# Performance work log

Measured on AMD Instinct MI355X. Metric: run time of the kernel, lower is better.

The kernel has to match this reference:

```python
import jax, jax.numpy as jnp
import numpy as np

SEQ, B, IN, H = 512, 64, 1024, 1024

def _lstm_layer(x_seq, Wx, bx, Wh, bh):
    # x_seq: [S, B, D], Wx: [4H, D], Wh: [4H, H]
    h0 = jnp.zeros((x_seq.shape[1], Wh.shape[1]), x_seq.dtype)
    c0 = jnp.zeros_like(h0)
    def step(carry, x_t):
        h, c = carry
        z = x_t @ Wx.T + bx + h @ Wh.T + bh  # [B, 4H]
        i, f, g, o = jnp.split(z, 4, axis=1)
        c1 = jax.nn.sigmoid(f) * c + jax.nn.sigmoid(i) * jnp.tanh(g)
        h1 = jax.nn.sigmoid(o) * jnp.tanh(c1)
        return (h1, c1), h1
    _, hs = jax.lax.scan(step, (h0, c0), x_seq)
    return hs  # [S, B, H]

def setup_inputs() -> dict:
    key = jax.random.key(0)
    ks = jax.random.split(key, 9)
    s_in = 1.0 / np.sqrt(IN)
    s_h = 1.0 / np.sqrt(H)
    return {
        "x": jax.random.normal(ks[0], (SEQ, B, IN), jnp.float32),
        "Wx0": jax.random.uniform(ks[1], (4 * H, IN), jnp.float32, -s_in, s_in),
        "bx0": jax.random.uniform(ks[2], (4 * H,), jnp.float32, -s_in, s_in),
        "Wh0": jax.random.uniform(ks[3], (4 * H, H), jnp.float32, -s_h, s_h),
        "bh0": jax.random.uniform(ks[4], (4 * H,), jnp.float32, -s_h, s_h),
        "Wx1": jax.random.uniform(ks[5], (4 * H, H), jnp.float32, -s_h, s_h),
        "bx1": jax.random.uniform(ks[6], (4 * H,), jnp.float32, -s_h, s_h),
        "Wh1": jax.random.uniform(ks[7], (4 * H, H), jnp.float32, -s_h, s_h),
        "bh1": jax.random.uniform(ks[8], (4 * H,), jnp.float32, -s_h, s_h),
    }

def reference(x, Wx0, bx0, Wh0, bh0, Wx1, bx1, Wh1, bh1):
    # Two stacked unidirectional LSTM layers, zero initial states.
    h_seq0 = _lstm_layer(x, Wx0, bx0, Wh0, bh0)
    h_seq1 = _lstm_layer(h_seq0, Wx1, bx1, Wh1, bh1)
    return h_seq1  # [S, B, H] = stacked version of the torch list output
```

## Files before the change

kernel.cpp:

```cpp
#include <hip/hip_runtime.h>


#define SEQ   512
#define BATCH 64
#define HID   1024
#define NG    4096
#define KCAT  2048
#define F0_BASE 0
#define E0_IDX  8192
#define F1_BASE 16384
#define E1_IDX  24576

#define SMEM_BYTES 133120

typedef __attribute__((ext_vector_type(8))) _Float16 f16x8;
typedef __attribute__((ext_vector_type(4))) _Float16 f16x4;
typedef __attribute__((ext_vector_type(4))) float    f32x4;

__device__ __forceinline__ float sigm_f(float x){ return 1.f/(1.f + __expf(-x)); }
__device__ __forceinline__ float tanh_f(float x){
    float e = __expf(-2.f*fabsf(x));
    float r = (1.f - e)/(1.f + e);
    return copysignf(r, x);
}

__device__ __forceinline__ void store_h8(_Float16* p, f16x4 v){
    asm volatile("global_store_dwordx2 %0, %1, off sc0 sc1" :: "v"(p), "v"(v) : "memory");
}
__device__ __forceinline__ void drain_vmem(){
    asm volatile("s_waitcnt vmcnt(0)" ::: "memory");
}

#define GLD(dst, base, OFF) \
    asm volatile("global_load_dwordx4 %0, %1, off offset:" #OFF \
                 : "=&v"(dst) : "v"(base))
#define GLD8L(arr, i, B) \
    GLD(arr[(i)+0],B,0);   GLD(arr[(i)+1],B,64);  GLD(arr[(i)+2],B,128); GLD(arr[(i)+3],B,192); \
    GLD(arr[(i)+4],B,256); GLD(arr[(i)+5],B,320); GLD(arr[(i)+6],B,384); GLD(arr[(i)+7],B,448)
#define GLD8H(arr, i, B) \
    GLD(arr[(i)+0],B,512); GLD(arr[(i)+1],B,576); GLD(arr[(i)+2],B,640); GLD(arr[(i)+3],B,704); \
    GLD(arr[(i)+4],B,768); GLD(arr[(i)+5],B,832); GLD(arr[(i)+6],B,896); GLD(arr[(i)+7],B,960)
#define VMWAIT0 \
    asm volatile("s_waitcnt vmcnt(0)" ::: "memory"); \
    __builtin_amdgcn_sched_barrier(0)


__global__ void prep_w_kernel(const float* __restrict__ Wx, const float* __restrict__ Wh,
                              const float* __restrict__ bx, const float* __restrict__ bh,
                              _Float16* __restrict__ Wr, float* __restrict__ br){
    int p = blockIdx.x;
    int j = p >> 2, g = p & 3;
    int r = g*1024 + j;
    int k = threadIdx.x * 8;
    const float* s = (k < 1024) ? (Wx + (size_t)r*1024 + k)
                                : (Wh + (size_t)r*1024 + (k - 1024));
    float4 v0 = *reinterpret_cast<const float4*>(s);
    float4 v1 = *reinterpret_cast<const float4*>(s + 4);
    f16x8 o;
    o[0]=(_Float16)v0.x; o[1]=(_Float16)v0.y; o[2]=(_Float16)v0.z; o[3]=(_Float16)v0.w;
    o[4]=(_Float16)v1.x; o[5]=(_Float16)v1.y; o[6]=(_Float16)v1.z; o[7]=(_Float16)v1.w;
    *reinterpret_cast<f16x8*>(Wr + (size_t)p*KCAT + k) = o;
    if (threadIdx.x == 0) br[p] = bx[r] + bh[r];
}

__global__ void prep_x_kernel(const float* __restrict__ x, _Float16* xo){
    size_t i = ((size_t)blockIdx.x*256 + threadIdx.x) * 8;
    float4 v0 = *reinterpret_cast<const float4*>(x + i);
    float4 v1 = *reinterpret_cast<const float4*>(x + i + 4);
    f16x8 o;
    o[0]=(_Float16)v0.x; o[1]=(_Float16)v0.y; o[2]=(_Float16)v0.z; o[3]=(_Float16)v0.w;
    o[4]=(_Float16)v1.x; o[5]=(_Float16)v1.y; o[6]=(_Float16)v1.z; o[7]=(_Float16)v1.w;
    *reinterpret_cast<f16x8*>(xo + i) = o;
}

__global__ void init_misc_kernel(int* flags, _Float16* hz){
    int i = blockIdx.x*256 + threadIdx.x;
    flags[i] = 0;
    if (i < 16384){
        f16x4 z; z[0]=(_Float16)0.f; z[1]=(_Float16)0.f; z[2]=(_Float16)0.f; z[3]=(_Float16)0.f;
        *reinterpret_cast<f16x4*>(hz + (size_t)i*4) = z;
    }
}


__device__ __forceinline__ void wait_epoch_g(const int* flags, int eidx, int k, int rep){
    for(;;){
        int e = __hip_atomic_load(&flags[eidx + rep*32], __ATOMIC_RELAXED, __HIP_MEMORY_SCOPE_AGENT);
        if (e >= k) break;
        __builtin_amdgcn_s_sleep(2);
    }
    asm volatile("" ::: "memory");
}

__device__ __forceinline__ void aggregate_publish(int* flags, int base, int eidx,
                                                  int k, int lane){
    const int b = lane*4;
    for(;;){
        int a0 = __hip_atomic_load(&flags[base + (b+0)*32], __ATOMIC_RELAXED, __HIP_MEMORY_SCOPE_AGENT);
        int a1 = __hip_atomic_load(&flags[base + (b+1)*32], __ATOMIC_RELAXED, __HIP_MEMORY_SCOPE_AGENT);
        int a2 = __hip_atomic_load(&flags[base + (b+2)*32], __ATOMIC_RELAXED, __HIP_MEMORY_SCOPE_AGENT);
        int a3 = __hip_atomic_load(&flags[base + (b+3)*32], __ATOMIC_RELAXED, __HIP_MEMORY_SCOPE_AGENT);
        bool ok = (a0>=k) && (a1>=k) && (a2>=k) && (a3>=k);
        if (__all(ok)) break;
        __builtin_amdgcn_s_sleep(1);
    }
    asm volatile("" ::: "memory");
    if (lane < 32)
        __hip_atomic_store(&flags[eidx + lane*32], k, __ATOMIC_RELAXED, __HIP_MEMORY_SCOPE_AGENT);
}


__device__ __forceinline__ f32x4 mfma16(f16x8 a, f16x8 b, f32x4 c){
    return __builtin_amdgcn_mfma_f32_16x16x32_f16(a, b, c, 0, 0, 0);
}

__device__ __forceinline__ void gemm_asm_ldsb(const _Float16* A, const char* wfrag,
                                              f32x4* acc){
    const _Float16* b0 = A;
    const _Float16* b1 = A + 16*1024;
    const _Float16* b2 = A + 32*1024;
    const _Float16* b3 = A + 48*1024;
    f16x8 a[32];
    __builtin_amdgcn_sched_barrier(0);
    GLD8L(a, 0, b0); GLD8L(a, 8, b1); GLD8L(a, 16, b2); GLD8L(a, 24, b3);
    VMWAIT0;
    #pragma unroll
    for (int kk = 0; kk < 8; ++kk){
        f16x8 bb = *reinterpret_cast<const f16x8*>(wfrag + kk*1024);
        acc[0] = mfma16(a[kk],      bb, acc[0]);
        acc[1] = mfma16(a[8 + kk],  bb, acc[1]);
        acc[2] = mfma16(a[16 + kk], bb, acc[2]);
        acc[3] = mfma16(a[24 + kk], bb, acc[3]);
    }
    __builtin_amdgcn_sched_barrier(0);
    GLD8H(a, 0, b0); GLD8H(a, 8, b1); GLD8H(a, 16, b2); GLD8H(a, 24, b3);
    VMWAIT0;
    #pragma unroll
    for (int kk = 0; kk < 8; ++kk){
        f16x8 bb = *reinterpret_cast<const f16x8*>(wfrag + (8 + kk)*1024);
        acc[0] = mfma16(a[kk],      bb, acc[0]);
        acc[1] = mfma16(a[8 + kk],  bb, acc[1]);
        acc[2] = mfma16(a[16 + kk], bb, acc[2]);
        acc[3] = mfma16(a[24 + kk], bb, acc[3]);
    }
    __builtin_amdgcn_sched_barrier(0);
}

__device__ __forceinline__ void gemm_asm_gb(const _Float16* A, const _Float16* Wp,
                                            f32x4* acc){
    const _Float16* b0 = A;
    const _Float16* b1 = A + 16*1024;
    const _Float16* b2 = A + 32*1024;
    const _Float16* b3 = A + 48*1024;
    f16x8 bw[8], a[32];
    __builtin_amdgcn_sched_barrier(0);
    GLD8L(bw, 0, Wp);
    GLD8L(a, 0, b0); GLD8L(a, 8, b1); GLD8L(a, 16, b2); GLD8L(a, 24, b3);
    VMWAIT0;
    #pragma unroll
    for (int kk = 0; kk < 8; ++kk){
        acc[0] = mfma16(a[kk],      bw[kk], acc[0]);
        acc[1] = mfma16(a[8 + kk],  bw[kk], acc[1]);
        acc[2] = mfma16(a[16 + kk], bw[kk], acc[2]);
        acc[3] = mfma16(a[24 + kk], bw[kk], acc[3]);
    }
    __builtin_amdgcn_sched_barrier(0);
    GLD8H(bw, 0, Wp);
    GLD8H(a, 0, b0); GLD8H(a, 8, b1); GLD8H(a, 16, b2); GLD8H(a, 24, b3);
    VMWAIT0;
    #pragma unroll
    for (int kk = 0; kk < 8; ++kk){
        acc[0] = mfma16(a[kk],      bw[kk], acc[0]);
        acc[1] = mfma16(a[8 + kk],  bw[kk], acc[1]);
        acc[2] = mfma16(a[16 + kk], bw[kk], acc[2]);
        acc[3] = mfma16(a[24 + kk], bw[kk], acc[3]);
    }
    __builtin_amdgcn_sched_barrier(0);
}

__device__ __forceinline__ void gemm_q_f32(const float* A, const _Float16* Wp, f32x4* acc){
    #pragma unroll 2
    for (int kk = 0; kk < 16; ++kk){
        f16x8 b = *reinterpret_cast<const f16x8*>(Wp + kk*32);
        f16x8 a[4];
        #pragma unroll
        for (int m = 0; m < 4; ++m){
            float4 u0 = *reinterpret_cast<const float4*>(A + kk*32 + (size_t)m*16*1024);
            float4 u1 = *reinterpret_cast<const float4*>(A + kk*32 + (size_t)m*16*1024 + 4);
            f16x8 v;
            v[0]=(_Float16)u0.x; v[1]=(_Float16)u0.y; v[2]=(_Float16)u0.z; v[3]=(_Float16)u0.w;
            v[4]=(_Float16)u1.x; v[5]=(_Float16)u1.y; v[6]=(_Float16)u1.z; v[7]=(_Float16)u1.w;
            a[m] = v;
        }
        acc[0] = mfma16(a[0], b, acc[0]);
        acc[1] = mfma16(a[1], b, acc[1]);
        acc[2] = mfma16(a[2], b, acc[2]);
        acc[3] = mfma16(a[3], b, acc[3]);
    }
}


__global__ __launch_bounds__(256, 1)
void lstm_persist(const _Float16* __restrict__ Wr0, const _Float16* __restrict__ Wr1,
                  const float* __restrict__ br0, const float* __restrict__ br1,
                  const _Float16* __restrict__ xbf, const float* __restrict__ xf32,
                  int use_xf16, const _Float16* __restrict__ hz,
                  _Float16* h0ring, _Float16* h1ring, float* out, int* flags){
    extern __shared__ char smem[];
    float (*accL)[4][64][17] = reinterpret_cast<float(*)[4][64][17]>(smem + 98304);

    const int tid  = threadIdx.x;
    const int wg   = blockIdx.x;
    const int wv   = tid >> 6;
    const int lane = tid & 63;
    const int r    = lane & 15;
    const int q    = lane >> 4;
    const int p0   = wg * 16;
    const int rep  = wg & 31;

    for (int idx = tid; idx < 6144; idx += 256){
        const _Float16* s; char* dst;
        if (idx < 2048){
            int wvh = idx >> 10, kk = (idx >> 6) & 15, ln = idx & 63;
            s = Wr0 + (size_t)(p0 + (ln & 15))*KCAT + 1024 + wvh*512 + kk*32 + (ln >> 4)*8;
            dst = smem + idx*16;
        } else {
            int d = idx - 2048;
            int wvd = d >> 10, kk = (d >> 6) & 15, ln = d & 63;
            s = Wr1 + (size_t)(p0 + (ln & 15))*KCAT + wvd*512 + kk*32 + (ln >> 4)*8;
            dst = smem + 32768 + d*16;
        }
        *reinterpret_cast<f16x8*>(dst) = *reinterpret_cast<const f16x8*>(s);
    }
    __syncthreads();

    f32x4 cst = {0.f,0.f,0.f,0.f};
    f32x4 ho_keep = {0.f,0.f,0.f,0.f};
    f32x4 bias[4];
    {
        const float* bsrc = (wv == 0) ? br0 : br1;
        #pragma unroll
        for (int jj = 0; jj < 4; ++jj)
            bias[jj] = *reinterpret_cast<const f32x4*>(&bsrc[p0 + jj*4]);
    }

    const int kofs = (wv & 1)*512 + q*8;
    const int wcol = wv*512 + q*8;
    const char* wh0frag = smem + (wv >= 2 ? (wv-2)*16384 : 0) + lane*16;
    const char* w1frag  = smem + 32768 + wv*16384 + lane*16;
    const size_t BH = (size_t)BATCH*HID;

    for (int k = 0; k <= SEQ; ++k){
        f32x4 acc[4];
        #pragma unroll
        for (int m = 0; m < 4; ++m){ acc[m].x=0;acc[m].y=0;acc[m].z=0;acc[m].w=0; }

        if (wv < 2){
            if (k < SEQ){
                if (use_xf16)
                    gemm_asm_gb(xbf + (size_t)k*BH + (size_t)r*HID + kofs,
                                Wr0 + (size_t)(p0 + r)*KCAT + wcol, acc);
                else
                    gemm_q_f32(xf32 + (size_t)k*BH + (size_t)r*HID + kofs,
                               Wr0 + (size_t)(p0 + r)*KCAT + wcol, acc);
            }
        } else {
            if (k > 0){
                if (wg == 0 && wv == 3) aggregate_publish(flags, F0_BASE, E0_IDX, k, lane);
                else                    wait_epoch_g(flags, E0_IDX, k, rep);
            }
            if (k < SEQ){
                const _Float16* A0 = (k == 0) ? (hz + (size_t)r*HID + kofs)
                                              : (h0ring + (size_t)(k-1)*BH + (size_t)r*HID + kofs);
                gemm_asm_ldsb(A0, wh0frag, acc);
            }
        }

        #pragma unroll
        for (int mt = 0; mt < 4; ++mt)
            #pragma unroll
            for (int j = 0; j < 4; ++j)
                accL[0][wv][mt*16 + q*4 + j][r] = acc[mt][j];
        __syncthreads();

        if (wv == 0 && k < SEQ){
            f32x4 zz[4];
            #pragma unroll
            for (int jj = 0; jj < 4; ++jj) zz[jj] = bias[jj];
            #pragma unroll
            for (int w2 = 0; w2 < 4; ++w2)
                #pragma unroll
                for (int jj = 0; jj < 4; ++jj){
                    f32x4 a = *reinterpret_cast<const f32x4*>(&accL[0][w2][lane][jj*4]);
                    zz[jj].x += a.x; zz[jj].y += a.y; zz[jj].z += a.z; zz[jj].w += a.w;
                }
            f16x4 hv;
            #pragma unroll
            for (int jl = 0; jl < 4; ++jl){
                float ig = sigm_f(zz[jl].x), fg = sigm_f(zz[jl].y);
                float gg = tanh_f(zz[jl].z), og = sigm_f(zz[jl].w);
                float c = fg*cst[jl] + ig*gg;  cst[jl] = c;
                hv[jl] = (_Float16)(og * tanh_f(c));
            }
            store_h8(h0ring + ((size_t)k*BATCH + lane)*HID + wg*4, hv);
            drain_vmem();
            if (lane == 0)
                __hip_atomic_store(&flags[F0_BASE + wg*32], k + 1,
                                   __ATOMIC_RELAXED, __HIP_MEMORY_SCOPE_AGENT);
        }

        #pragma unroll
        for (int m = 0; m < 4; ++m){ acc[m].x=0;acc[m].y=0;acc[m].z=0;acc[m].w=0; }

        if (k >= 1){
            if (wv < 2){
                gemm_asm_ldsb(h0ring + (size_t)(k-1)*BH + (size_t)r*HID + kofs,
                              w1frag, acc);
            } else {
                if (k >= 2){
                    if (wg == 0 && wv == 2) aggregate_publish(flags, F1_BASE, E1_IDX, k-1, lane);
                    else                    wait_epoch_g(flags, E1_IDX, k-1, rep);
                }
                const _Float16* A1 = (k == 1) ? (hz + (size_t)r*HID + kofs)
                                              : (h1ring + (size_t)(k-2)*BH + (size_t)r*HID + kofs);
                gemm_asm_ldsb(A1, w1frag, acc);
            }
        }

        #pragma unroll
        for (int mt = 0; mt < 4; ++mt)
            #pragma unroll
            for (int j = 0; j < 4; ++j)
                accL[1][wv][mt*16 + q*4 + j][r] = acc[mt][j];
        __syncthreads();

        if (wv == 1 && k >= 1){
            const int t1 = k - 1;
            f32x4 zz[4];
            #pragma unroll
            for (int jj = 0; jj < 4; ++jj) zz[jj] = bias[jj];
            #pragma unroll
            for (int w2 = 0; w2 < 4; ++w2)
                #pragma unroll
                for (int jj = 0; jj < 4; ++jj){
                    f32x4 a = *reinterpret_cast<const f32x4*>(&accL[1][w2][lane][jj*4]);
                    zz[jj].x += a.x; zz[jj].y += a.y; zz[jj].z += a.z; zz[jj].w += a.w;
                }
            f16x4 hv; f32x4 ho;
            #pragma unroll
            for (int jl = 0; jl < 4; ++jl){
                float ig = sigm_f(zz[jl].x), fg = sigm_f(zz[jl].y);
                float gg = tanh_f(zz[jl].z), og = sigm_f(zz[jl].w);
                float c = fg*cst[jl] + ig*gg;  cst[jl] = c;
                float h = og * tanh_f(c);
                hv[jl] = (_Float16)h;  ho[jl] = h;
            }
            if (k < SEQ) store_h8(h1ring + ((size_t)t1*BATCH + lane)*HID + wg*4, hv);
            if (t1 < SEQ-1) *reinterpret_cast<f32x4*>(out + ((size_t)t1*BATCH + lane)*HID + wg*4) = ho;
            else            ho_keep = ho;
            drain_vmem();
            if (lane == 0)
                __hip_atomic_store(&flags[F1_BASE + wg*32], k,
                                   __ATOMIC_RELAXED, __HIP_MEMORY_SCOPE_AGENT);
        }
    }

    if (tid == 0)
        __hip_atomic_store(&flags[F0_BASE + wg*32], SEQ + 1,
                           __ATOMIC_RELAXED, __HIP_MEMORY_SCOPE_AGENT);
    if (wg == 0 && wv == 3) aggregate_publish(flags, F0_BASE, E0_IDX, SEQ + 1, lane);
    if (wv == 1){
        wait_epoch_g(flags, E0_IDX, SEQ + 1, rep);
        *reinterpret_cast<f32x4*>(out + ((size_t)(SEQ-1)*BATCH + lane)*HID + wg*4) = ho_keep;
    }
}


extern "C" void kernel_launch(void* const* d_in, const int* in_sizes, int n_in,
                              void* d_out, int out_size, void* d_ws, size_t ws_size,
                              hipStream_t stream){
    const float* x   = (const float*)d_in[0];
    const float* Wx0 = (const float*)d_in[1];
    const float* bx0 = (const float*)d_in[2];
    const float* Wh0 = (const float*)d_in[3];
    const float* bh0 = (const float*)d_in[4];
    const float* Wx1 = (const float*)d_in[5];
    const float* bx1 = (const float*)d_in[6];
    const float* Wh1 = (const float*)d_in[7];
    const float* bh1 = (const float*)d_in[8];
    float* out = (float*)d_out;
    char* ws = (char*)d_ws;

    size_t o = 0;
    _Float16* Wr0 = (_Float16*)(ws + o); o += (size_t)NG*KCAT*2;
    _Float16* Wr1 = (_Float16*)(ws + o); o += (size_t)NG*KCAT*2;
    float* br0 = (float*)(ws + o); o += 16384;
    float* br1 = (float*)(ws + o); o += 16384;
    _Float16* h1ring = (_Float16*)(ws + o); o += (size_t)SEQ*BATCH*HID*2;
    _Float16* hz     = (_Float16*)(ws + o); o += (size_t)BATCH*HID*2;
    int* flags = (int*)(ws + o); o += 131072;

    const size_t RING = (size_t)SEQ*BATCH*HID*2;
    _Float16 *xbf = nullptr, *h0ring;
    int use_xf16 = 0;
    if (ws_size >= o + 2*RING){
        xbf    = (_Float16*)(ws + o);  o += RING;  use_xf16 = 1;
        h0ring = (_Float16*)(ws + o);  o += RING;
    } else if (ws_size >= o + RING){
        xbf    = (_Float16*)(ws + o);  o += RING;  use_xf16 = 1;
        h0ring = (_Float16*)((char*)d_out + (size_t)64*1024*1024);
    } else {
        h0ring = (_Float16*)((char*)d_out + (size_t)64*1024*1024);
    }

    hipFuncSetAttribute((const void*)lstm_persist,
                        hipFuncAttributeMaxDynamicSharedMemorySize, SMEM_BYTES);

    prep_w_kernel<<<NG, 256, 0, stream>>>(Wx0, Wh0, bx0, bh0, Wr0, br0);
    prep_w_kernel<<<NG, 256, 0, stream>>>(Wx1, Wh1, bx1, bh1, Wr1, br1);
    if (use_xf16)
        prep_x_kernel<<<(SEQ*BATCH*HID)/(256*8), 256, 0, stream>>>(x, xbf);
    init_misc_kernel<<<128, 256, 0, stream>>>(flags, hz);
    lstm_persist<<<256, 256, SMEM_BYTES, stream>>>(Wr0, Wr1, br0, br1, xbf, x, use_xf16,
                                                   hz, h0ring, h1ring, out, flags);
}
```

Baseline: 8.766 ms.

## Split LSTM layers across separate workgroup sets in persistent kernel

Launches 512 workgroups instead of 256. The first 256 run layer 0 and the second 256 run layer 1, each pipelined through global flags rather than interleaved in one workgroup. LDS per block is halved, and the gate epilogue is spread across all four waves instead of one, which means scalar half-precision stores. This allows layer-1 work to overlap with layer-0 steps and adds parallelism. The risks are that 512 persistent blocks must all be co-resident to avoid deadlock, and that the extra flag synchronisation and narrower stores add overhead.

```diff
diff --git a/kernel.cpp b/kernel.cpp
--- a/kernel.cpp
+++ b/kernel.cpp
@@ -11,10 +11,10 @@
 #define F1_BASE 16384
 #define E1_IDX  24576
 
-#define SMEM_BYTES 133120
+#define ACC_OFF  49152
+#define SMEM_BYTES 66560
 
 typedef __attribute__((ext_vector_type(8))) _Float16 f16x8;
-typedef __attribute__((ext_vector_type(4))) _Float16 f16x4;
 typedef __attribute__((ext_vector_type(4))) float    f32x4;
 
 __device__ __forceinline__ float sigm_f(float x){ return 1.f/(1.f + __expf(-x)); }
@@ -24,8 +24,8 @@
     return copysignf(r, x);
 }
 
-__device__ __forceinline__ void store_h8(_Float16* p, f16x4 v){
-    asm volatile("global_store_dwordx2 %0, %1, off sc0 sc1" :: "v"(p), "v"(v) : "memory");
+__device__ __forceinline__ void store_h2(_Float16* p, unsigned v){
+    asm volatile("global_store_short %0, %1, off sc0 sc1" :: "v"(p), "v"(v) : "memory");
 }
 __device__ __forceinline__ void drain_vmem(){
     asm volatile("s_waitcnt vmcnt(0)" ::: "memory");
@@ -77,6 +77,7 @@
     int i = blockIdx.x*256 + threadIdx.x;
     flags[i] = 0;
     if (i < 16384){
+        typedef __attribute__((ext_vector_type(4))) _Float16 f16x4;
         f16x4 z; z[0]=(_Float16)0.f; z[1]=(_Float16)0.f; z[2]=(_Float16)0.f; z[3]=(_Float16)0.f;
         *reinterpret_cast<f16x4*>(hz + (size_t)i*4) = z;
     }
@@ -207,172 +208,146 @@
                   int use_xf16, const _Float16* __restrict__ hz,
                   _Float16* h0ring, _Float16* h1ring, float* out, int* flags){
     extern __shared__ char smem[];
-    float (*accL)[4][64][17] = reinterpret_cast<float(*)[4][64][17]>(smem + 98304);
-
-    const int tid  = threadIdx.x;
-    const int wg   = blockIdx.x;
-    const int wv   = tid >> 6;
-    const int lane = tid & 63;
-    const int r    = lane & 15;
-    const int q    = lane >> 4;
-    const int p0   = wg * 16;
-    const int rep  = wg & 31;
-
-    for (int idx = tid; idx < 6144; idx += 256){
-        const _Float16* s; char* dst;
-        if (idx < 2048){
+    float (*accL)[64][17] = reinterpret_cast<float(*)[64][17]>(smem + ACC_OFF);
+
+    const int tid   = threadIdx.x;
+    const int wgid  = blockIdx.x;
+    const int layer = wgid >> 8;
+    const int wgl   = wgid & 255;
+    const int wv    = tid >> 6;
+    const int lane  = tid & 63;
+    const int r     = lane & 15;
+    const int q     = lane >> 4;
+    const int p0    = wgl * 16;
+    const int rep   = wgl & 31;
+    const size_t BH = (size_t)BATCH*HID;
+
+    if (layer == 0){
+        for (int idx = tid; idx < 2048; idx += 256){
             int wvh = idx >> 10, kk = (idx >> 6) & 15, ln = idx & 63;
-            s = Wr0 + (size_t)(p0 + (ln & 15))*KCAT + 1024 + wvh*512 + kk*32 + (ln >> 4)*8;
-            dst = smem + idx*16;
-        } else {
-            int d = idx - 2048;
-            int wvd = d >> 10, kk = (d >> 6) & 15, ln = d & 63;
-            s = Wr1 + (size_t)(p0 + (ln & 15))*KCAT + wvd*512 + kk*32 + (ln >> 4)*8;
-            dst = smem + 32768 + d*16;
-        }
-        *reinterpret_cast<f16x8*>(dst) = *reinterpret_cast<const f16x8*>(s);
+            const _Float16* s = Wr0 + (size_t)(p0 + (ln & 15))*KCAT + 1024
+                                + wvh*512 + kk*32 + (ln >> 4)*8;
+            *reinterpret_cast<f16x8*>(smem + idx*16) = *reinterpret_cast<const f16x8*>(s);
+        }
+    } else {
+        for (int idx = tid; idx < 3072; idx += 256){
+            int wvd = idx >> 10, kk = (idx >> 6) & 15, ln = idx & 63;
+            const _Float16* s = Wr1 + (size_t)(p0 + (ln & 15))*KCAT + 512
+                                + wvd*512 + kk*32 + (ln >> 4)*8;
+            *reinterpret_cast<f16x8*>(smem + idx*16) = *reinterpret_cast<const f16x8*>(s);
+        }
     }
     __syncthreads();
-
-    f32x4 cst = {0.f,0.f,0.f,0.f};
-    f32x4 ho_keep = {0.f,0.f,0.f,0.f};
-    f32x4 bias[4];
-    {
-        const float* bsrc = (wv == 0) ? br0 : br1;
-        #pragma unroll
-        for (int jj = 0; jj < 4; ++jj)
-            bias[jj] = *reinterpret_cast<const f32x4*>(&bsrc[p0 + jj*4]);
-    }
 
     const int kofs = (wv & 1)*512 + q*8;
     const int wcol = wv*512 + q*8;
-    const char* wh0frag = smem + (wv >= 2 ? (wv-2)*16384 : 0) + lane*16;
-    const char* w1frag  = smem + 32768 + wv*16384 + lane*16;
-    const size_t BH = (size_t)BATCH*HID;
-
-    for (int k = 0; k <= SEQ; ++k){
-        f32x4 acc[4];
-        #pragma unroll
-        for (int m = 0; m < 4; ++m){ acc[m].x=0;acc[m].y=0;acc[m].z=0;acc[m].w=0; }
-
-        if (wv < 2){
-            if (k < SEQ){
+    float cst = 0.f, ho_keep = 0.f;
+    f32x4 bias = *reinterpret_cast<const f32x4*>(&(layer ? br1 : br0)[p0 + wv*4]);
+
+    if (layer == 0){
+        const char* wfrag = smem + (wv >= 2 ? (wv-2)*16384 : 0) + lane*16;
+        for (int k = 0; k < SEQ; ++k){
+            f32x4 acc[4];
+            #pragma unroll
+            for (int m = 0; m < 4; ++m){ acc[m].x=0;acc[m].y=0;acc[m].z=0;acc[m].w=0; }
+
+            if (wv < 2){
                 if (use_xf16)
                     gemm_asm_gb(xbf + (size_t)k*BH + (size_t)r*HID + kofs,
                                 Wr0 + (size_t)(p0 + r)*KCAT + wcol, acc);
                 else
                     gemm_q_f32(xf32 + (size_t)k*BH + (size_t)r*HID + kofs,
                                Wr0 + (size_t)(p0 + r)*KCAT + wcol, acc);
-            }
-        } else {
-            if (k > 0){
-                if (wg == 0 && wv == 3) aggregate_publish(flags, F0_BASE, E0_IDX, k, lane);
-                else                    wait_epoch_g(flags, E0_IDX, k, rep);
-            }
-            if (k < SEQ){
+            } else {
+                if (k > 0) wait_epoch_g(flags, E0_IDX, k, rep);
                 const _Float16* A0 = (k == 0) ? (hz + (size_t)r*HID + kofs)
                                               : (h0ring + (size_t)(k-1)*BH + (size_t)r*HID + kofs);
-                gemm_asm_ldsb(A0, wh0frag, acc);
+                gemm_asm_ldsb(A0, wfrag, acc);
             }
+
+            #pragma unroll
+            for (int mt = 0; mt < 4; ++mt)
+                #pragma unroll
+                for (int j = 0; j < 4; ++j)
+                    accL[wv][mt*16 + q*4 + j][r] = acc[mt][j];
+            __syncthreads();
+
+            f32x4 z = bias;
+            #pragma unroll
+            for (int w2 = 0; w2 < 4; ++w2){
+                f32x4 a = *reinterpret_cast<const f32x4*>(&accL[w2][lane][wv*4]);
+                z.x += a.x; z.y += a.y; z.z += a.z; z.w += a.w;
+            }
+            float c = sigm_f(z.y)*cst + sigm_f(z.x)*tanh_f(z.z);
+            cst = c;
+            _Float16 hh = (_Float16)(sigm_f(z.w) * tanh_f(c));
+            unsigned hb = (unsigned)__builtin_bit_cast(unsigned short, hh);
+            store_h2(h0ring + ((size_t)k*BATCH + lane)*HID + wgl*4 + wv, hb);
+            drain_vmem();
+            __syncthreads();
+            if (tid == 0)
+                __hip_atomic_store(&flags[F0_BASE + wgl*32], k + 1,
+                                   __ATOMIC_RELAXED, __HIP_MEMORY_SCOPE_AGENT);
+        }
+        return;
+    }
+
+    const char* wfrag = smem + (wv >= 1 ? (wv-1)*16384 : 0) + lane*16;
+    for (int k = 1; k <= SEQ; ++k){
+        const int t1 = k - 1;
+        f32x4 acc[4];
+        #pragma unroll
+        for (int m = 0; m < 4; ++m){ acc[m].x=0;acc[m].y=0;acc[m].z=0;acc[m].w=0; }
+
+        if (wv < 2){
+            if (wv == 0 && wgl == 0) aggregate_publish(flags, F0_BASE, E0_IDX, k, lane);
+            else                     wait_epoch_g(flags, E0_IDX, k, rep);
+            const _Float16* A = h0ring + (size_t)(k-1)*BH + (size_t)r*HID + kofs;
+            if (wv == 0)
+                gemm_asm_gb(A, Wr1 + (size_t)(p0 + r)*KCAT + q*8, acc);
+            else
+                gemm_asm_ldsb(A, wfrag, acc);
+        } else {
+            if (k >= 2){
+                if (wv == 2 && wgl == 1) aggregate_publish(flags, F1_BASE, E1_IDX, k-1, lane);
+                else                     wait_epoch_g(flags, E1_IDX, k-1, rep);
+            }
+            const _Float16* A = (k == 1) ? (hz + (size_t)r*HID + kofs)
+                                         : (h1ring + (size_t)(k-2)*BH + (size_t)r*HID + kofs);
+            gemm_asm_ldsb(A, wfrag, acc);
         }
 
         #pragma unroll
         for (int mt = 0; mt < 4; ++mt)
             #pragma unroll
             for (int j = 0; j < 4; ++j)
-                accL[0][wv][mt*16 + q*4 + j][r] = acc[mt][j];
+                accL[wv][mt*16 + q*4 + j][r] = acc[mt][j];
         __syncthreads();
 
-        if (wv == 0 && k < SEQ){
-            f32x4 zz[4];
-            #pragma unroll
-            for (int jj = 0; jj < 4; ++jj) zz[jj] = bias[jj];
-            #pragma unroll
-            for (int w2 = 0; w2 < 4; ++w2)
-                #pragma unroll
-                for (int jj = 0; jj < 4; ++jj){
-                    f32x4 a = *reinterpret_cast<const f32x4*>(&accL[0][w2][lane][jj*4]);
-                    zz[jj].x += a.x; zz[jj].y += a.y; zz[jj].z += a.z; zz[jj].w += a.w;
-                }
-            f16x4 hv;
-            #pragma unroll
-            for (int jl = 0; jl < 4; ++jl){
-                float ig = sigm_f(zz[jl].x), fg = sigm_f(zz[jl].y);
-                float gg = tanh_f(zz[jl].z), og = sigm_f(zz[jl].w);
-                float c = fg*cst[jl] + ig*gg;  cst[jl] = c;
-                hv[jl] = (_Float16)(og * tanh_f(c));
-            }
-            store_h8(h0ring + ((size_t)k*BATCH + lane)*HID + wg*4, hv);
-            drain_vmem();
-            if (lane == 0)
-                __hip_atomic_store(&flags[F0_BASE + wg*32], k + 1,
-                                   __ATOMIC_RELAXED, __HIP_MEMORY_SCOPE_AGENT);
-        }
-
+        f32x4 z = bias;
         #pragma unroll
-        for (int m = 0; m < 4; ++m){ acc[m].x=0;acc[m].y=0;acc[m].z=0;acc[m].w=0; }
-
-        if (k >= 1){
-            if (wv < 2){
-                gemm_asm_ldsb(h0ring + (size_t)(k-1)*BH + (size_t)r*HID + kofs,
-                              w1frag, acc);
-            } else {
-                if (k >= 2){
-                    if (wg == 0 && wv == 2) aggregate_publish(flags, F1_BASE, E1_IDX, k-1, lane);
-                    else                    wait_epoch_g(flags, E1_IDX, k-1, rep);
-                }
-                const _Float16* A1 = (k == 1) ? (hz + (size_t)r*HID + kofs)
-                                              : (h1ring + (size_t)(k-2)*BH + (size_t)r*HID + kofs);
-                gemm_asm_ldsb(A1, w1frag, acc);
-            }
-        }
-
-        #pragma unroll
-        for (int mt = 0; mt < 4; ++mt)
-            #pragma unroll
-            for (int j = 0; j < 4; ++j)
-                accL[1][wv][mt*16 + q*4 + j][r] = acc[mt][j];
+        for (int w2 = 0; w2 < 4; ++w2){
+            f32x4 a = *reinterpret_cast<const f32x4*>(&accL[w2][lane][wv*4]);
+            z.x += a.x; z.y += a.y; z.z += a.z; z.w += a.w;
+        }
+        float c = sigm_f(z.y)*cst + sigm_f(z.x)*tanh_f(z.z);
+        cst = c;
+        float h = sigm_f(z.w) * tanh_f(c);
+        _Float16 hh = (_Float16)h;
+        unsigned hb = (unsigned)__builtin_bit_cast(unsigned short, hh);
+        store_h2(h1ring + ((size_t)t1*BATCH + lane)*HID + wgl*4 + wv, hb);
+        if (t1 < SEQ-1) out[((size_t)t1*BATCH + lane)*HID + wgl*4 + wv] = h;
+        else            ho_keep = h;
+        drain_vmem();
         __syncthreads();
-
-        if (wv == 1 && k >= 1){
-            const int t1 = k - 1;
-            f32x4 zz[4];
-            #pragma unroll
-            for (int jj = 0; jj < 4; ++jj) zz[jj] = bias[jj];
-            #pragma unroll
-            for (int w2 = 0; w2 < 4; ++w2)
-                #pragma unroll
-                for (int jj = 0; jj < 4; ++jj){
-                    f32x4 a = *reinterpret_cast<const f32x4*>(&accL[1][w2][lane][jj*4]);
-                    zz[jj].x += a.x; zz[jj].y += a.y; zz[jj].z += a.z; zz[jj].w += a.w;
-                }
-            f16x4 hv; f32x4 ho;
-            #pragma unroll
-            for (int jl = 0; jl < 4; ++jl){
-                float ig = sigm_f(zz[jl].x), fg = sigm_f(zz[jl].y);
-                float gg = tanh_f(zz[jl].z), og = sigm_f(zz[jl].w);
-                float c = fg*cst[jl] + ig*gg;  cst[jl] = c;
-                float h = og * tanh_f(c);
-                hv[jl] = (_Float16)h;  ho[jl] = h;
-            }
-            if (k < SEQ) store_h8(h1ring + ((size_t)t1*BATCH + lane)*HID + wg*4, hv);
-            if (t1 < SEQ-1) *reinterpret_cast<f32x4*>(out + ((size_t)t1*BATCH + lane)*HID + wg*4) = ho;
-            else            ho_keep = ho;
-            drain_vmem();
-            if (lane == 0)
-                __hip_atomic_store(&flags[F1_BASE + wg*32], k,
-                                   __ATOMIC_RELAXED, __HIP_MEMORY_SCOPE_AGENT);
-        }
-    }
-
-    if (tid == 0)
-        __hip_atomic_store(&flags[F0_BASE + wg*32], SEQ + 1,
-                           __ATOMIC_RELAXED, __HIP_MEMORY_SCOPE_AGENT);
-    if (wg == 0 && wv == 3) aggregate_publish(flags, F0_BASE, E0_IDX, SEQ + 1, lane);
-    if (wv == 1){
-        wait_epoch_g(flags, E0_IDX, SEQ + 1, rep);
-        *reinterpret_cast<f32x4*>(out + ((size_t)(SEQ-1)*BATCH + lane)*HID + wg*4) = ho_keep;
-    }
+        if (tid == 0)
+            __hip_atomic_store(&flags[F1_BASE + wgl*32], k,
+                               __ATOMIC_RELAXED, __HIP_MEMORY_SCOPE_AGENT);
+    }
+
+    if (wgl == 1 && wv == 2) aggregate_publish(flags, F1_BASE, E1_IDX, SEQ, lane);
+    wait_epoch_g(flags, E1_IDX, SEQ, rep);
+    out[((size_t)(SEQ-1)*BATCH + lane)*HID + wgl*4 + wv] = ho_keep;
 }
 
 
@@ -421,6 +396,6 @@
     if (use_xf16)
         prep_x_kernel<<<(SEQ*BATCH*HID)/(256*8), 256, 0, stream>>>(x, xbf);
     init_misc_kernel<<<128, 256, 0, stream>>>(flags, hz);
-    lstm_persist<<<256, 256, SMEM_BYTES, stream>>>(Wr0, Wr1, br0, br1, xbf, x, use_xf16,
+    lstm_persist<<<512, 256, SMEM_BYTES, stream>>>(Wr0, Wr1, br0, br1, xbf, x, use_xf16,
                                                    hz, h0ring, h1ring, out, flags);
 }
```

New measurement: 9.926 ms. +13.2%, slower.

## Add dedicated aggregator wave to publish grid-barrier epochs for both layers

Applied to the files above, without the earlier changes.

Adds a fifth wave per workgroup. In workgroup 0 it continuously scans the per-block progress flags for both layers and publishes the minimum epochs, so compute waves no longer stall while aggregating. A shared-memory mark lets the aggregator track which phase the block is in, and the extra wave in the other blocks only matches the barrier calls. This takes aggregation off the critical path of waves 2 and 3, at the cost of an extra wave per CU and more polling traffic on the flags.

```diff
diff --git a/kernel.cpp b/kernel.cpp
--- a/kernel.cpp
+++ b/kernel.cpp
@@ -11,7 +11,8 @@
 #define F1_BASE 16384
 #define E1_IDX  24576
 
-#define SMEM_BYTES 133120
+#define MARK_OFF 133120
+#define SMEM_BYTES 133184
 
 typedef __attribute__((ext_vector_type(8))) _Float16 f16x8;
 typedef __attribute__((ext_vector_type(4))) _Float16 f16x4;
@@ -83,9 +84,16 @@
 }
 
 
+__device__ __forceinline__ int gload(const int* p){
+    return __hip_atomic_load(p, __ATOMIC_RELAXED, __HIP_MEMORY_SCOPE_AGENT);
+}
+__device__ __forceinline__ void gstore(int* p, int v){
+    __hip_atomic_store(p, v, __ATOMIC_RELAXED, __HIP_MEMORY_SCOPE_AGENT);
+}
+
 __device__ __forceinline__ void wait_epoch_g(const int* flags, int eidx, int k, int rep){
     for(;;){
-        int e = __hip_atomic_load(&flags[eidx + rep*32], __ATOMIC_RELAXED, __HIP_MEMORY_SCOPE_AGENT);
+        int e = gload(&flags[eidx + rep*32]);
         if (e >= k) break;
         __builtin_amdgcn_s_sleep(2);
     }
@@ -96,17 +104,47 @@
                                                   int k, int lane){
     const int b = lane*4;
     for(;;){
-        int a0 = __hip_atomic_load(&flags[base + (b+0)*32], __ATOMIC_RELAXED, __HIP_MEMORY_SCOPE_AGENT);
-        int a1 = __hip_atomic_load(&flags[base + (b+1)*32], __ATOMIC_RELAXED, __HIP_MEMORY_SCOPE_AGENT);
-        int a2 = __hip_atomic_load(&flags[base + (b+2)*32], __ATOMIC_RELAXED, __HIP_MEMORY_SCOPE_AGENT);
-        int a3 = __hip_atomic_load(&flags[base + (b+3)*32], __ATOMIC_RELAXED, __HIP_MEMORY_SCOPE_AGENT);
+        int a0 = gload(&flags[base + (b+0)*32]);
+        int a1 = gload(&flags[base + (b+1)*32]);
+        int a2 = gload(&flags[base + (b+2)*32]);
+        int a3 = gload(&flags[base + (b+3)*32]);
         bool ok = (a0>=k) && (a1>=k) && (a2>=k) && (a3>=k);
         if (__all(ok)) break;
         __builtin_amdgcn_s_sleep(1);
     }
     asm volatile("" ::: "memory");
     if (lane < 32)
-        __hip_atomic_store(&flags[eidx + lane*32], k, __ATOMIC_RELAXED, __HIP_MEMORY_SCOPE_AGENT);
+        gstore(&flags[eidx + lane*32], k);
+}
+
+__device__ __forceinline__ int wave_min_i(int v){
+    #pragma unroll
+    for (int off = 1; off < 64; off <<= 1)
+        v = min(v, __shfl_xor(v, off));
+    return v;
+}
+
+__device__ __forceinline__ void scan_publish(int* flags, int lane, int& pub0, int& pub1){
+    int f0 = 0x7fffffff, f1 = 0x7fffffff;
+    #pragma unroll
+    for (int j = 0; j < 4; ++j){
+        int i4 = lane*4 + j;
+        f0 = min(f0, gload(&flags[F0_BASE + i4*32]));
+        f1 = min(f1, gload(&flags[F1_BASE + i4*32]));
+    }
+    int m0 = wave_min_i(f0), m1 = wave_min_i(f1);
+    if (m0 > pub0){ if (lane < 32) gstore(&flags[E0_IDX + lane*32], m0); pub0 = m0; }
+    if (m1 > pub1){ if (lane < 32) gstore(&flags[E1_IDX + lane*32], m1); pub1 = m1; }
+}
+
+__device__ __forceinline__ void agg_window(int* flags, int* mark, int tgt,
+                                           int& pub0, int& pub1, int lane){
+    while (__hip_atomic_load(mark, __ATOMIC_RELAXED, __HIP_MEMORY_SCOPE_WORKGROUP) < tgt){
+        scan_publish(flags, lane, pub0, pub1);
+        __builtin_amdgcn_s_sleep(1);
+    }
+    scan_publish(flags, lane, pub0, pub1);
+    asm volatile("" ::: "memory");
 }
 
 
@@ -200,7 +238,7 @@
 }
 
 
-__global__ __launch_bounds__(256, 1)
+__global__ __launch_bounds__(320, 1)
 void lstm_persist(const _Float16* __restrict__ Wr0, const _Float16* __restrict__ Wr1,
                   const float* __restrict__ br0, const float* __restrict__ br1,
                   const _Float16* __restrict__ xbf, const float* __restrict__ xf32,
@@ -208,6 +246,7 @@
                   _Float16* h0ring, _Float16* h1ring, float* out, int* flags){
     extern __shared__ char smem[];
     float (*accL)[4][64][17] = reinterpret_cast<float(*)[4][64][17]>(smem + 98304);
+    int* mark = reinterpret_cast<int*>(smem + MARK_OFF);
 
     const int tid  = threadIdx.x;
     const int wg   = blockIdx.x;
@@ -218,7 +257,7 @@
     const int p0   = wg * 16;
     const int rep  = wg & 31;
 
-    for (int idx = tid; idx < 6144; idx += 256){
+    for (int idx = tid; idx < 6144; idx += 320){
         const _Float16* s; char* dst;
         if (idx < 2048){
             int wvh = idx >> 10, kk = (idx >> 6) & 15, ln = idx & 63;
@@ -232,7 +271,27 @@
         }
         *reinterpret_cast<f16x8*>(dst) = *reinterpret_cast<const f16x8*>(s);
     }
+    if (tid == 0) *mark = 0;
     __syncthreads();
+
+    if (wv == 4){
+        if (wg == 0){
+            int pub0 = 0, pub1 = 0;
+            for (int k = 0; k <= SEQ; ++k){
+                agg_window(flags, mark, 2*k + 1, pub0, pub1, lane);
+                __syncthreads();
+                agg_window(flags, mark, 2*k + 2, pub0, pub1, lane);
+                __syncthreads();
+            }
+            aggregate_publish(flags, F0_BASE, E0_IDX, SEQ + 1, lane);
+        } else {
+            for (int k = 0; k <= SEQ; ++k){
+                __syncthreads();
+                __syncthreads();
+            }
+        }
+        return;
+    }
 
     f32x4 cst = {0.f,0.f,0.f,0.f};
     f32x4 ho_keep = {0.f,0.f,0.f,0.f};
@@ -265,10 +324,7 @@
                                Wr0 + (size_t)(p0 + r)*KCAT + wcol, acc);
             }
         } else {
-            if (k > 0){
-                if (wg == 0 && wv == 3) aggregate_publish(flags, F0_BASE, E0_IDX, k, lane);
-                else                    wait_epoch_g(flags, E0_IDX, k, rep);
-            }
+            if (k > 0) wait_epoch_g(flags, E0_IDX, k, rep);
             if (k < SEQ){
                 const _Float16* A0 = (k == 0) ? (hz + (size_t)r*HID + kofs)
                                               : (h0ring + (size_t)(k-1)*BH + (size_t)r*HID + kofs);
@@ -281,6 +337,8 @@
             #pragma unroll
             for (int j = 0; j < 4; ++j)
                 accL[0][wv][mt*16 + q*4 + j][r] = acc[mt][j];
+        if (wv == 3 && lane == 0)
+            __hip_atomic_store(mark, 2*k + 1, __ATOMIC_RELAXED, __HIP_MEMORY_SCOPE_WORKGROUP);
         __syncthreads();
 
         if (wv == 0 && k < SEQ){
@@ -304,9 +362,7 @@
             }
             store_h8(h0ring + ((size_t)k*BATCH + lane)*HID + wg*4, hv);
             drain_vmem();
-            if (lane == 0)
-                __hip_atomic_store(&flags[F0_BASE + wg*32], k + 1,
-                                   __ATOMIC_RELAXED, __HIP_MEMORY_SCOPE_AGENT);
+            if (lane == 0) gstore(&flags[F0_BASE + wg*32], k + 1);
         }
 
         #pragma unroll
@@ -317,10 +373,7 @@
                 gemm_asm_ldsb(h0ring + (size_t)(k-1)*BH + (size_t)r*HID + kofs,
                               w1frag, acc);
             } else {
-                if (k >= 2){
-                    if (wg == 0 && wv == 2) aggregate_publish(flags, F1_BASE, E1_IDX, k-1, lane);
-                    else                    wait_epoch_g(flags, E1_IDX, k-1, rep);
-                }
+                if (k >= 2) wait_epoch_g(flags, E1_IDX, k-1, rep);
                 const _Float16* A1 = (k == 1) ? (hz + (size_t)r*HID + kofs)
                                               : (h1ring + (size_t)(k-2)*BH + (size_t)r*HID + kofs);
                 gemm_asm_ldsb(A1, w1frag, acc);
@@ -332,6 +385,8 @@
             #pragma unroll
             for (int j = 0; j < 4; ++j)
                 accL[1][wv][mt*16 + q*4 + j][r] = acc[mt][j];
+        if (wv == 3 && lane == 0)
+            __hip_atomic_store(mark, 2*k + 2, __ATOMIC_RELAXED, __HIP_MEMORY_SCOPE_WORKGROUP);
         __syncthreads();
 
         if (wv == 1 && k >= 1){
@@ -359,16 +414,11 @@
             if (t1 < SEQ-1) *reinterpret_cast<f32x4*>(out + ((size_t)t1*BATCH + lane)*HID + wg*4) = ho;
             else            ho_keep = ho;
             drain_vmem();
-            if (lane == 0)
-                __hip_atomic_store(&flags[F1_BASE + wg*32], k,
-                                   __ATOMIC_RELAXED, __HIP_MEMORY_SCOPE_AGENT);
-        }
-    }
-
-    if (tid == 0)
-        __hip_atomic_store(&flags[F0_BASE + wg*32], SEQ + 1,
-                           __ATOMIC_RELAXED, __HIP_MEMORY_SCOPE_AGENT);
-    if (wg == 0 && wv == 3) aggregate_publish(flags, F0_BASE, E0_IDX, SEQ + 1, lane);
+            if (lane == 0) gstore(&flags[F1_BASE + wg*32], k);
+        }
+    }
+
+    if (tid == 0) gstore(&flags[F0_BASE + wg*32], SEQ + 1);
     if (wv == 1){
         wait_epoch_g(flags, E0_IDX, SEQ + 1, rep);
         *reinterpret_cast<f32x4*>(out + ((size_t)(SEQ-1)*BATCH + lane)*HID + wg*4) = ho_keep;
@@ -421,6 +471,6 @@
     if (use_xf16)
         prep_x_kernel<<<(SEQ*BATCH*HID)/(256*8), 256, 0, stream>>>(x, xbf);
     init_misc_kernel<<<128, 256, 0, stream>>>(flags, hz);
-    lstm_persist<<<256, 256, SMEM_BYTES, stream>>>(Wr0, Wr1, br0, br1, xbf, x, use_xf16,
+    lstm_persist<<<256, 320, SMEM_BYTES, stream>>>(Wr0, Wr1, br0, br1, xbf, x, use_xf16,
                                                    hz, h0ring, h1ring, out, flags);
 }
```

After: 9.279 ms. 5.9% more time.

## Run both LSTM layers concurrently with 8 waves and a single merged grid barrier

Applied to the files above, without the earlier changes.

Doubles the persistent block from 4 to 8 waves so layer-0 and layer-1 GEMM work for a step run in parallel on separate waves instead of one after the other. The two per-step grid barriers (one per layer) become one combined epoch: a single aggregator waits on both layers' flags and publishes one epoch value. The aim is fewer global synchronisation round-trips per step and more overlap between the layers. In exchange each wave does half the work and there are extra __syncthreads, so register pressure under 512-thread launch bounds and the coupling of both layers to the slower one are the risks.

```diff
diff --git a/kernel.cpp b/kernel.cpp
--- a/kernel.cpp
+++ b/kernel.cpp
@@ -7,9 +7,8 @@
 #define NG    4096
 #define KCAT  2048
 #define F0_BASE 0
-#define E0_IDX  8192
-#define F1_BASE 16384
-#define E1_IDX  24576
+#define F1_BASE 8192
+#define E_IDX   16384
 
 #define SMEM_BYTES 133120
 
@@ -83,30 +82,38 @@
 }
 
 
-__device__ __forceinline__ void wait_epoch_g(const int* flags, int eidx, int k, int rep){
+__device__ __forceinline__ int gload(const int* p){
+    return __hip_atomic_load(p, __ATOMIC_RELAXED, __HIP_MEMORY_SCOPE_AGENT);
+}
+__device__ __forceinline__ void gstore(int* p, int v){
+    __hip_atomic_store(p, v, __ATOMIC_RELAXED, __HIP_MEMORY_SCOPE_AGENT);
+}
+
+__device__ __forceinline__ void wait_epoch_g(const int* flags, int k, int rep){
     for(;;){
-        int e = __hip_atomic_load(&flags[eidx + rep*32], __ATOMIC_RELAXED, __HIP_MEMORY_SCOPE_AGENT);
+        int e = gload(&flags[E_IDX + rep*32]);
         if (e >= k) break;
         __builtin_amdgcn_s_sleep(2);
     }
     asm volatile("" ::: "memory");
 }
 
-__device__ __forceinline__ void aggregate_publish(int* flags, int base, int eidx,
-                                                  int k, int lane){
+__device__ __forceinline__ void aggregate_publish_dual(int* flags, int k, int lane){
     const int b = lane*4;
     for(;;){
-        int a0 = __hip_atomic_load(&flags[base + (b+0)*32], __ATOMIC_RELAXED, __HIP_MEMORY_SCOPE_AGENT);
-        int a1 = __hip_atomic_load(&flags[base + (b+1)*32], __ATOMIC_RELAXED, __HIP_MEMORY_SCOPE_AGENT);
-        int a2 = __hip_atomic_load(&flags[base + (b+2)*32], __ATOMIC_RELAXED, __HIP_MEMORY_SCOPE_AGENT);
-        int a3 = __hip_atomic_load(&flags[base + (b+3)*32], __ATOMIC_RELAXED, __HIP_MEMORY_SCOPE_AGENT);
-        bool ok = (a0>=k) && (a1>=k) && (a2>=k) && (a3>=k);
+        int m = 0x7fffffff;
+        #pragma unroll
+        for (int j = 0; j < 4; ++j){
+            m = min(m, gload(&flags[F0_BASE + (b+j)*32]));
+            m = min(m, gload(&flags[F1_BASE + (b+j)*32]));
+        }
+        bool ok = (m >= k);
         if (__all(ok)) break;
         __builtin_amdgcn_s_sleep(1);
     }
     asm volatile("" ::: "memory");
     if (lane < 32)
-        __hip_atomic_store(&flags[eidx + lane*32], k, __ATOMIC_RELAXED, __HIP_MEMORY_SCOPE_AGENT);
+        gstore(&flags[E_IDX + lane*32], k);
 }
 
 
@@ -200,7 +207,7 @@
 }
 
 
-__global__ __launch_bounds__(256, 1)
+__global__ __launch_bounds__(512, 1)
 void lstm_persist(const _Float16* __restrict__ Wr0, const _Float16* __restrict__ Wr1,
                   const float* __restrict__ br0, const float* __restrict__ br1,
                   const _Float16* __restrict__ xbf, const float* __restrict__ xf32,
@@ -217,8 +224,10 @@
     const int q    = lane >> 4;
     const int p0   = wg * 16;
     const int rep  = wg & 31;
-
-    for (int idx = tid; idx < 6144; idx += 256){
+    const int kh   = wv & 1;
+    const size_t BH = (size_t)BATCH*HID;
+
+    for (int idx = tid; idx < 6144; idx += 512){
         const _Float16* s; char* dst;
         if (idx < 2048){
             int wvh = idx >> 10, kk = (idx >> 6) & 15, ln = idx & 63;
@@ -244,43 +253,56 @@
             bias[jj] = *reinterpret_cast<const f32x4*>(&bsrc[p0 + jj*4]);
     }
 
-    const int kofs = (wv & 1)*512 + q*8;
-    const int wcol = wv*512 + q*8;
-    const char* wh0frag = smem + (wv >= 2 ? (wv-2)*16384 : 0) + lane*16;
-    const char* w1frag  = smem + 32768 + wv*16384 + lane*16;
-    const size_t BH = (size_t)BATCH*HID;
+    const int kofs = kh*512 + q*8;
+    const char* wfrag =
+        (wv < 4) ? (smem + kh*16384 + lane*16)
+                 : (wv < 6) ? (smem + 32768 + kh*16384 + lane*16)
+                            : (smem + 65536 + kh*16384 + lane*16);
 
     for (int k = 0; k <= SEQ; ++k){
         f32x4 acc[4];
         #pragma unroll
         for (int m = 0; m < 4; ++m){ acc[m].x=0;acc[m].y=0;acc[m].z=0;acc[m].w=0; }
 
+        if (k > 0){
+            if (wg == 0 && wv == 0)      aggregate_publish_dual(flags, k, lane);
+            else if (wv >= 2 && wv < 6)  wait_epoch_g(flags, k, rep);
+            else if (wv >= 6 && k >= 2)  wait_epoch_g(flags, k, rep);
+        }
+
         if (wv < 2){
             if (k < SEQ){
                 if (use_xf16)
                     gemm_asm_gb(xbf + (size_t)k*BH + (size_t)r*HID + kofs,
-                                Wr0 + (size_t)(p0 + r)*KCAT + wcol, acc);
+                                Wr0 + (size_t)(p0 + r)*KCAT + kh*512 + q*8, acc);
                 else
                     gemm_q_f32(xf32 + (size_t)k*BH + (size_t)r*HID + kofs,
-                               Wr0 + (size_t)(p0 + r)*KCAT + wcol, acc);
+                               Wr0 + (size_t)(p0 + r)*KCAT + kh*512 + q*8, acc);
             }
+        } else if (wv < 4){
+            if (k < SEQ){
+                const _Float16* A = (k == 0) ? (hz + (size_t)r*HID + kofs)
+                                             : (h0ring + (size_t)(k-1)*BH + (size_t)r*HID + kofs);
+                gemm_asm_ldsb(A, wfrag, acc);
+            }
+        } else if (wv < 6){
+            if (k >= 1)
+                gemm_asm_ldsb(h0ring + (size_t)(k-1)*BH + (size_t)r*HID + kofs, wfrag, acc);
         } else {
-            if (k > 0){
-                if (wg == 0 && wv == 3) aggregate_publish(flags, F0_BASE, E0_IDX, k, lane);
-                else                    wait_epoch_g(flags, E0_IDX, k, rep);
+            if (k >= 1){
+                const _Float16* A = (k == 1) ? (hz + (size_t)r*HID + kofs)
+                                             : (h1ring + (size_t)(k-2)*BH + (size_t)r*HID + kofs);
+                gemm_asm_ldsb(A, wfrag, acc);
             }
-            if (k < SEQ){
-                const _Float16* A0 = (k == 0) ? (hz + (size_t)r*HID + kofs)
-                                              : (h0ring + (size_t)(k-1)*BH + (size_t)r*HID + kofs);
-                gemm_asm_ldsb(A0, wh0frag, acc);
-            }
-        }
+        }
+
+        __syncthreads();
 
         #pragma unroll
         for (int mt = 0; mt < 4; ++mt)
             #pragma unroll
             for (int j = 0; j < 4; ++j)
-                accL[0][wv][mt*16 + q*4 + j][r] = acc[mt][j];
+                accL[wv >> 2][wv & 3][mt*16 + q*4 + j][r] = acc[mt][j];
         __syncthreads();
 
         if (wv == 0 && k < SEQ){
@@ -288,10 +310,10 @@
             #pragma unroll
             for (int jj = 0; jj < 4; ++jj) zz[jj] = bias[jj];
             #pragma unroll
-            for (int w2 = 0; w2 < 4; ++w2)
+            for (int c = 0; c < 4; ++c)
                 #pragma unroll
                 for (int jj = 0; jj < 4; ++jj){
-                    f32x4 a = *reinterpret_cast<const f32x4*>(&accL[0][w2][lane][jj*4]);
+                    f32x4 a = *reinterpret_cast<const f32x4*>(&accL[0][c][lane][jj*4]);
                     zz[jj].x += a.x; zz[jj].y += a.y; zz[jj].z += a.z; zz[jj].w += a.w;
                 }
             f16x4 hv;
@@ -304,73 +326,44 @@
             }
             store_h8(h0ring + ((size_t)k*BATCH + lane)*HID + wg*4, hv);
             drain_vmem();
-            if (lane == 0)
-                __hip_atomic_store(&flags[F0_BASE + wg*32], k + 1,
-                                   __ATOMIC_RELAXED, __HIP_MEMORY_SCOPE_AGENT);
-        }
-
-        #pragma unroll
-        for (int m = 0; m < 4; ++m){ acc[m].x=0;acc[m].y=0;acc[m].z=0;acc[m].w=0; }
-
-        if (k >= 1){
-            if (wv < 2){
-                gemm_asm_ldsb(h0ring + (size_t)(k-1)*BH + (size_t)r*HID + kofs,
-                              w1frag, acc);
-            } else {
-                if (k >= 2){
-                    if (wg == 0 && wv == 2) aggregate_publish(flags, F1_BASE, E1_IDX, k-1, lane);
-                    else                    wait_epoch_g(flags, E1_IDX, k-1, rep);
+            if (lane == 0) gstore(&flags[F0_BASE + wg*32], k + 1);
+        }
+
+        if (wv == 4){
+            if (k >= 1){
+                const int t1 = k - 1;
+                f32x4 zz[4];
+                #pragma unroll
+                for (int jj = 0; jj < 4; ++jj) zz[jj] = bias[jj];
+                #pragma unroll
+                for (int c = 0; c < 4; ++c)
+                    #pragma unroll
+                    for (int jj = 0; jj < 4; ++jj){
+                        f32x4 a = *reinterpret_cast<const f32x4*>(&accL[1][c][lane][jj*4]);
+                        zz[jj].x += a.x; zz[jj].y += a.y; zz[jj].z += a.z; zz[jj].w += a.w;
+                    }
+                f16x4 hv; f32x4 ho;
+                #pragma unroll
+                for (int jl = 0; jl < 4; ++jl){
+                    float ig = sigm_f(zz[jl].x), fg = sigm_f(zz[jl].y);
+                    float gg = tanh_f(zz[jl].z), og = sigm_f(zz[jl].w);
+                    float c = fg*cst[jl] + ig*gg;  cst[jl] = c;
+                    float h = og * tanh_f(c);
+                    hv[jl] = (_Float16)h;  ho[jl] = h;
                 }
-                const _Float16* A1 = (k == 1) ? (hz + (size_t)r*HID + kofs)
-                                              : (h1ring + (size_t)(k-2)*BH + (size_t)r*HID + kofs);
-                gemm_asm_ldsb(A1, w1frag, acc);
+                if (k < SEQ) store_h8(h1ring + ((size_t)t1*BATCH + lane)*HID + wg*4, hv);
+                if (t1 < SEQ-1) *reinterpret_cast<f32x4*>(out + ((size_t)t1*BATCH + lane)*HID + wg*4) = ho;
+                else            ho_keep = ho;
+                drain_vmem();
             }
-        }
-
-        #pragma unroll
-        for (int mt = 0; mt < 4; ++mt)
-            #pragma unroll
-            for (int j = 0; j < 4; ++j)
-                accL[1][wv][mt*16 + q*4 + j][r] = acc[mt][j];
-        __syncthreads();
-
-        if (wv == 1 && k >= 1){
-            const int t1 = k - 1;
-            f32x4 zz[4];
-            #pragma unroll
-            for (int jj = 0; jj < 4; ++jj) zz[jj] = bias[jj];
-            #pragma unroll
-            for (int w2 = 0; w2 < 4; ++w2)
-                #pragma unroll
-                for (int jj = 0; jj < 4; ++jj){
-                    f32x4 a = *reinterpret_cast<const f32x4*>(&accL[1][w2][lane][jj*4]);
-                    zz[jj].x += a.x; zz[jj].y += a.y; zz[jj].z += a.z; zz[jj].w += a.w;
-                }
-            f16x4 hv; f32x4 ho;
-            #pragma unroll
-            for (int jl = 0; jl < 4; ++jl){
-                float ig = sigm_f(zz[jl].x), fg = sigm_f(zz[jl].y);
-                float gg = tanh_f(zz[jl].z), og = sigm_f(zz[jl].w);
-                float c = fg*cst[jl] + ig*gg;  cst[jl] = c;
-                float h = og * tanh_f(c);
-                hv[jl] = (_Float16)h;  ho[jl] = h;
-            }
-            if (k < SEQ) store_h8(h1ring + ((size_t)t1*BATCH + lane)*HID + wg*4, hv);
-            if (t1 < SEQ-1) *reinterpret_cast<f32x4*>(out + ((size_t)t1*BATCH + lane)*HID + wg*4) = ho;
-            else            ho_keep = ho;
-            drain_vmem();
-            if (lane == 0)
-                __hip_atomic_store(&flags[F1_BASE + wg*32], k,
-                                   __ATOMIC_RELAXED, __HIP_MEMORY_SCOPE_AGENT);
-        }
-    }
-
-    if (tid == 0)
-        __hip_atomic_store(&flags[F0_BASE + wg*32], SEQ + 1,
-                           __ATOMIC_RELAXED, __HIP_MEMORY_SCOPE_AGENT);
-    if (wg == 0 && wv == 3) aggregate_publish(flags, F0_BASE, E0_IDX, SEQ + 1, lane);
-    if (wv == 1){
-        wait_epoch_g(flags, E0_IDX, SEQ + 1, rep);
+            if (lane == 0) gstore(&flags[F1_BASE + wg*32], k + 1);
+        }
+    }
+
+    if (tid == 0) gstore(&flags[F0_BASE + wg*32], SEQ + 1);
+    if (wg == 0 && wv == 0) aggregate_publish_dual(flags, SEQ + 1, lane);
+    if (wv == 4){
+        wait_epoch_g(flags, SEQ + 1, rep);
         *reinterpret_cast<f32x4*>(out + ((size_t)(SEQ-1)*BATCH + lane)*HID + wg*4) = ho_keep;
     }
 }
@@ -421,6 +414,6 @@
     if (use_xf16)
         prep_x_kernel<<<(SEQ*BATCH*HID)/(256*8), 256, 0, stream>>>(x, xbf);
     init_misc_kernel<<<128, 256, 0, stream>>>(flags, hz);
-    lstm_persist<<<256, 256, SMEM_BYTES, stream>>>(Wr0, Wr1, br0, br1, xbf, x, use_xf16,
+    lstm_persist<<<256, 512, SMEM_BYTES, stream>>>(Wr0, Wr1, br0, br1, xbf, x, use_xf16,
                                                    hz, h0ring, h1ring, out, flags);
 }
```

Measured after the change: 9.699 ms. 10.6% more time.
